# Kernel tuning notes

Hardware: AMD Instinct MI355X
Metric: run time of the kernel (lower is better)

The kernel has to match this reference:

```python
import jax, jax.numpy as jnp
from jax import lax
import numpy as np

H = 256      # encoder_hidden
F = 256      # variance predictor filter_size
K = 3        # kernel_size
NBINS = 256  # variance_embedding n_bins
B, S, T = 64, 512, 2048


def conv1d(x, w, b, pad):
    # x: [B, L, Cin], w: [K, Cin, Cout] -> [B, L, Cout]
    y = lax.conv_general_dilated(x, w, window_strides=(1,), padding=[(pad, pad)],
                                 dimension_numbers=('NWC', 'WIO', 'NWC'))
    return y + b


def layer_norm(x, g, b, eps=1e-5):
    mu = jnp.mean(x, -1, keepdims=True)
    v = jnp.mean((x - mu) ** 2, -1, keepdims=True)
    return (x - mu) * lax.rsqrt(v + eps) * g + b


def predictor(x, mask, w1, b1, g1, be1, w2, b2, g2, be2, lw, lb):
    h = jax.nn.relu(conv1d(x, w1, b1, (K - 1) // 2))
    h = layer_norm(h, g1, be1)
    h = jax.nn.relu(conv1d(h, w2, b2, 1))  # padding=1 hardcoded in original conv1d_2
    h = layer_norm(h, g2, be2)
    out = (h @ lw + lb)[..., 0]            # [B, L]
    return jnp.where(mask, 0.0, out)       # masked_fill(mask, 0.0)


def setup_inputs():
    key = jax.random.key(0)
    ks = jax.random.split(key, 16)
    inp = {
        'x': jax.random.normal(ks[0], (B, S, H), jnp.float32),
        'pitch_target': jax.random.normal(ks[1], (B, S), jnp.float32),
        'energy_target': jax.random.normal(ks[2], (B, S), jnp.float32),
        'src_mask': jnp.zeros((B, S), bool),
        'duration': jax.random.randint(ks[3], (B, S), 0, 4, jnp.int32),
        'max_len': T,
    }
    i = 4
    for p in ['d', 'p', 'e']:
        inp[p + '_w1'] = jax.random.normal(ks[i], (K, H, F), jnp.float32) * 0.05; i += 1
        inp[p + '_b1'] = jnp.zeros((F,), jnp.float32)
        inp[p + '_g1'] = jnp.ones((F,), jnp.float32)
        inp[p + '_be1'] = jnp.zeros((F,), jnp.float32)
        inp[p + '_w2'] = jax.random.normal(ks[i], (K, F, F), jnp.float32) * 0.05; i += 1
        inp[p + '_b2'] = jnp.zeros((F,), jnp.float32)
        inp[p + '_g2'] = jnp.ones((F,), jnp.float32)
        inp[p + '_be2'] = jnp.zeros((F,), jnp.float32)
        inp[p + '_lw'] = jax.random.normal(ks[i], (F, 1), jnp.float32) * 0.05; i += 1
        inp[p + '_lb'] = jnp.zeros((1,), jnp.float32)
    inp['p_table'] = jax.random.normal(ks[i], (NBINS, H), jnp.float32) * 0.02; i += 1
    inp['e_table'] = jax.random.normal(ks[i], (NBINS, H), jnp.float32) * 0.02
    return inp


def reference(x, pitch_target, energy_target, src_mask, duration, max_len,
              d_w1, d_b1, d_g1, d_be1, d_w2, d_b2, d_g2, d_be2, d_lw, d_lb,
              p_w1, p_b1, p_g1, p_be1, p_w2, p_b2, p_g2, p_be2, p_lw, p_lb,
              e_w1, e_b1, e_g1, e_be1, e_w2, e_b2, e_g2, e_be2, e_lw, e_lb,
              p_table, e_table):
    # linear-quantized bins over the data range (stats.json min/max -> [-2, 2] for randn data)
    bins = jnp.linspace(-2.0, 2.0, NBINS - 1, dtype=jnp.float32)

    log_d_pred = predictor(x, src_mask, d_w1, d_b1, d_g1, d_be1, d_w2, d_b2, d_g2, d_be2, d_lw, d_lb)

    # phoneme-level pitch (training path: target given -> embed bucketized target)
    p_pred = predictor(x, src_mask, p_w1, p_b1, p_g1, p_be1, p_w2, p_b2, p_g2, p_be2, p_lw, p_lb)
    p_emb = p_table[jnp.searchsorted(bins, pitch_target, side='left')]  # torch.bucketize(right=False)
    x = x + p_emb

    # phoneme-level energy (predictor runs on x AFTER pitch embedding, as in original)
    e_pred = predictor(x, src_mask, e_w1, e_b1, e_g1, e_be1, e_w2, e_b2, e_g2, e_be2, e_lw, e_lb)
    e_emb = e_table[jnp.searchsorted(bins, energy_target, side='left')]
    x = x + e_emb

    # Length regulation: expand phoneme i duration[b, i] times, pad to max_len.
    cum = jnp.cumsum(duration, axis=1)                 # [B, S]
    mel_len = cum[:, -1]                               # [B]
    frames = jnp.arange(max_len)                       # [T]
    # frame t maps to first phoneme i with cum[i] > t
    idx = jax.vmap(lambda c: jnp.searchsorted(c, frames, side='right'))(cum)  # [B, T]
    idx = jnp.minimum(idx, duration.shape[1] - 1)
    mel = jnp.take_along_axis(x, idx[:, :, None], axis=1)                     # [B, T, H]
    valid = frames[None, :] < mel_len[:, None]
    mel = jnp.where(valid[:, :, None], mel, 0.0)       # zero-pad beyond mel_len

    d_rounded = duration
    return (mel, p_pred, e_pred, log_d_pred, d_rounded, mel_len)
```

## Files before the change

kernel.cpp:

```cpp
#include <hip/hip_runtime.h>
#include <cstdint>
#include <cstddef>


#define HH 256
#define SS 512
#define BB 64
#define TT 2048
#define LSTR 264

typedef __bf16 bf16;
typedef __attribute__((ext_vector_type(8))) __bf16 bf16x8;
typedef __attribute__((ext_vector_type(4))) __bf16 bf16x4;
typedef __attribute__((ext_vector_type(4))) float f32x4;

static constexpr size_t WSZ  = (size_t)3 * HH * HH;
static constexpr size_t H1SZ = (size_t)BB * SS * HH;

__device__ __forceinline__ float edge_val(int j) {
    const float step = 4.0f / 254.0f;
    if (j == 254) return 2.0f;
    return __fadd_rn(-2.0f, __fmul_rn((float)j, step));
}
__device__ __forceinline__ int bucket256(float v) {
    int lo = 0, hi = 255;
    while (lo < hi) {
        int mid = (lo + hi) >> 1;
        if (edge_val(mid) < v) lo = mid + 1; else hi = mid;
    }
    return lo;
}

__global__ void wt_pack(const float* __restrict__ w0, const float* __restrict__ w1,
                        const float* __restrict__ w2, const float* __restrict__ w3,
                        const float* __restrict__ w4, const float* __restrict__ w5,
                        bf16* __restrict__ wp) {
    const int cv = blockIdx.x / 3, k = blockIdx.x % 3;
    const float* wsel[6] = {w0, w1, w2, w3, w4, w5};
    const float* wk = wsel[cv] + (size_t)k * HH * HH;
    bf16* o = wp + ((size_t)(cv * 3 + k)) * HH * HH;
    for (int fb = 0; fb < 16; ++fb) {
        #pragma unroll
        for (int h = 0; h < 2; ++h) {
            const int idx  = threadIdx.x + 256 * h;
            const int kcb  = idx >> 6, lane = idx & 63;
            const int f    = fb * 16 + (lane & 15);
            const int c0   = kcb * 32 + (lane >> 4) * 8;
            bf16x8 v;
            #pragma unroll
            for (int j = 0; j < 8; ++j) v[j] = (bf16)wk[(size_t)(c0 + j) * HH + f];
            *(bf16x8*)(o + (((size_t)fb * 8 + kcb) * 64 + lane) * 8) = v;
        }
    }
}

__global__ __launch_bounds__(256) void xcvt_kernel(
    const float* __restrict__ x, const float* __restrict__ pt,
    const float* __restrict__ ptab,
    bf16* __restrict__ x1, bf16* __restrict__ x2)
{
    const int row = blockIdx.x * 8 + (threadIdx.x >> 5);
    const int c   = (threadIdx.x & 31) * 8;
    const int pb  = bucket256(pt[row]);
    const float4 v0 = *(const float4*)(x + (size_t)row * HH + c);
    const float4 v1 = *(const float4*)(x + (size_t)row * HH + c + 4);
    const float4 t0 = *(const float4*)(ptab + (size_t)pb * HH + c);
    const float4 t1 = *(const float4*)(ptab + (size_t)pb * HH + c + 4);
    bf16x8 a, b2;
    a[0] = (bf16)v0.x; a[1] = (bf16)v0.y; a[2] = (bf16)v0.z; a[3] = (bf16)v0.w;
    a[4] = (bf16)v1.x; a[5] = (bf16)v1.y; a[6] = (bf16)v1.z; a[7] = (bf16)v1.w;
    b2[0] = (bf16)(v0.x + t0.x); b2[1] = (bf16)(v0.y + t0.y);
    b2[2] = (bf16)(v0.z + t0.z); b2[3] = (bf16)(v0.w + t0.w);
    b2[4] = (bf16)(v1.x + t1.x); b2[5] = (bf16)(v1.y + t1.y);
    b2[6] = (bf16)(v1.z + t1.z); b2[7] = (bf16)(v1.w + t1.w);
    *(bf16x8*)(x1 + (size_t)row * HH + c) = a;
    *(bf16x8*)(x2 + (size_t)row * HH + c) = b2;
}

struct Args3 {
    const float* bias[3];
    const float* g[3];
    const float* be[3];
    const float* lw[3];
    const float* lb[3];
    float*       out[3];
};

__global__ __launch_bounds__(256, 3) void conv_fused(
    const bf16* __restrict__ x1,
    const bf16* __restrict__ x2,
    const bf16* __restrict__ wpk,
    Args3 a1, Args3 a2,
    const uint8_t* __restrict__ mask)
{
    __shared__ alignas(16) bf16 tile[82 * LSTR];
    __shared__ float red_s[80][4], red_q[80][4];
    __shared__ float ln_m[80], ln_r[80];

    const int tid    = threadIdx.x;
    const int pred   = blockIdx.x >> 9;
    const int within = blockIdx.x & 511;
    const int b      = within >> 3;
    const int s0     = (within & 7) * 64;

    const int lane = tid & 63;
    const int wv   = tid >> 6;

    const bf16* inb = (pred == 2 ? x2 : x1) + (size_t)b * SS * HH;
    const bf16* wt1 = wpk + (size_t)(pred * 2) * WSZ;
    const bf16* wt2 = wt1 + WSZ;

    for (int idx = tid; idx < 82 * 32; idx += 256) {
        const int r   = idx >> 5, c16 = idx & 31;
        const int s   = s0 - 9 + r;
        bf16x8 v = {};
        if (s >= 0 && s < SS)
            v = *(const bf16x8*)(inb + (size_t)s * HH + c16 * 8);
        *(bf16x8*)&tile[r * LSTR + c16 * 8] = v;
    }
    __syncthreads();

    const int ln15 = lane & 15;
    const int g8   = (lane >> 4) << 3;
    const int q4   = (lane >> 4) << 2;

    f32x4 bini[4];
    #pragma unroll
    for (int mf = 0; mf < 4; ++mf)
        #pragma unroll
        for (int i = 0; i < 4; ++i)
            bini[mf][i] = a1.bias[pred][64 * wv + 16 * mf + q4 + i];

    f32x4 acc1[4][5];
    #pragma unroll
    for (int mf = 0; mf < 4; ++mf)
        #pragma unroll
        for (int sf = 0; sf < 5; ++sf) acc1[mf][sf] = bini[mf];

    #pragma unroll 2
    for (int t = 0; t < 24; ++t) {
        const int k = t >> 3, kcb = t & 7;
        const int kc = kcb << 5;
        bf16x8 aw[4], bx[5];
        const bf16* bp = wt1 + ((((size_t)k * 16 + wv * 4) * 8 + kcb) << 9)
                       + (size_t)lane * 8;
        #pragma unroll
        for (int mf = 0; mf < 4; ++mf)
            aw[mf] = *(const bf16x8*)(bp + ((size_t)mf << 12));
        #pragma unroll
        for (int sf = 0; sf < 5; ++sf)
            bx[sf] = *(const bf16x8*)&tile[(16 * sf + ln15 + k) * LSTR + kc + g8];
        #pragma unroll
        for (int mf = 0; mf < 4; ++mf)
            #pragma unroll
            for (int sf = 0; sf < 5; ++sf)
                acc1[mf][sf] = __builtin_amdgcn_mfma_f32_16x16x32_bf16(
                    aw[mf], bx[sf], acc1[mf][sf], 0, 0, 0);
    }

    #pragma unroll
    for (int mf = 0; mf < 4; ++mf)
        #pragma unroll
        for (int sf = 0; sf < 5; ++sf)
            #pragma unroll
            for (int i = 0; i < 4; ++i)
                acc1[mf][sf][i] = fmaxf(acc1[mf][sf][i], 0.f);

    #pragma unroll
    for (int sf = 0; sf < 5; ++sf) {
        float s = 0.f, q = 0.f;
        #pragma unroll
        for (int mf = 0; mf < 4; ++mf)
            #pragma unroll
            for (int i = 0; i < 4; ++i) {
                const float v = acc1[mf][sf][i];
                s += v; q += v * v;
            }
        s += __shfl_xor(s, 16); s += __shfl_xor(s, 32);
        q += __shfl_xor(q, 16); q += __shfl_xor(q, 32);
        if (lane < 16) { red_s[16 * sf + lane][wv] = s; red_q[16 * sf + lane][wv] = q; }
    }
    __syncthreads();
    if (tid < 80) {
        const float s = red_s[tid][0] + red_s[tid][1] + red_s[tid][2] + red_s[tid][3];
        const float q = red_q[tid][0] + red_q[tid][1] + red_q[tid][2] + red_q[tid][3];
        const float mean = s * (1.f / 256.f);
        const float var  = q * (1.f / 256.f) - mean * mean;
        ln_m[tid] = mean;
        ln_r[tid] = rsqrtf(var + 1e-5f);
    }
    __syncthreads();

    {
        float g1v[4][4], be1v[4][4];
        #pragma unroll
        for (int mf = 0; mf < 4; ++mf)
            #pragma unroll
            for (int i = 0; i < 4; ++i) {
                const int f1 = 64 * wv + 16 * mf + q4 + i;
                g1v[mf][i]  = a1.g[pred][f1];
                be1v[mf][i] = a1.be[pred][f1];
            }
        #pragma unroll
        for (int sf = 0; sf < 5; ++sf) {
            const int o  = 16 * sf + ln15;
            const int hr = o - 7;
            const float mean = ln_m[o], rs = ln_r[o];
            const bool ok = (o >= 7 && o <= 72);
            #pragma unroll
            for (int mf = 0; mf < 4; ++mf) {
                bf16x4 hv;
                #pragma unroll
                for (int i = 0; i < 4; ++i)
                    hv[i] = (bf16)((acc1[mf][sf][i] - mean) * rs * g1v[mf][i] + be1v[mf][i]);
                if (ok)
                    *(bf16x4*)&tile[hr * LSTR + 64 * wv + 16 * mf + q4] = hv;
            }
        }
    }
    __syncthreads();
    if (tid < 64) {
        if (s0 == 0)       *(uint2*)&tile[tid * 4]            = make_uint2(0u, 0u);
        if (s0 == SS - 64) *(uint2*)&tile[65 * LSTR + tid * 4] = make_uint2(0u, 0u);
    }
    __syncthreads();

    #pragma unroll
    for (int mf = 0; mf < 4; ++mf)
        #pragma unroll
        for (int i = 0; i < 4; ++i)
            bini[mf][i] = a2.bias[pred][64 * wv + 16 * mf + q4 + i];

    f32x4 acc2[4][4];
    #pragma unroll
    for (int mf = 0; mf < 4; ++mf)
        #pragma unroll
        for (int sf = 0; sf < 4; ++sf) acc2[mf][sf] = bini[mf];

    #pragma unroll 2
    for (int t = 0; t < 24; ++t) {
        const int k = t >> 3, kcb = t & 7;
        const int kc = kcb << 5;
        bf16x8 aw[4], bx[4];
        const bf16* bp = wt2 + ((((size_t)k * 16 + wv * 4) * 8 + kcb) << 9)
                       + (size_t)lane * 8;
        #pragma unroll
        for (int mf = 0; mf < 4; ++mf)
            aw[mf] = *(const bf16x8*)(bp + ((size_t)mf << 12));
        #pragma unroll
        for (int sf = 0; sf < 4; ++sf)
            bx[sf] = *(const bf16x8*)&tile[(16 * sf + ln15 + k) * LSTR + kc + g8];
        #pragma unroll
        for (int mf = 0; mf < 4; ++mf)
            #pragma unroll
            for (int sf = 0; sf < 4; ++sf)
                acc2[mf][sf] = __builtin_amdgcn_mfma_f32_16x16x32_bf16(
                    aw[mf], bx[sf], acc2[mf][sf], 0, 0, 0);
    }

    #pragma unroll
    for (int mf = 0; mf < 4; ++mf)
        #pragma unroll
        for (int sf = 0; sf < 4; ++sf)
            #pragma unroll
            for (int i = 0; i < 4; ++i)
                acc2[mf][sf][i] = fmaxf(acc2[mf][sf][i], 0.f);

    #pragma unroll
    for (int sf = 0; sf < 4; ++sf) {
        float s = 0.f, q = 0.f;
        #pragma unroll
        for (int mf = 0; mf < 4; ++mf)
            #pragma unroll
            for (int i = 0; i < 4; ++i) {
                const float v = acc2[mf][sf][i];
                s += v; q += v * v;
            }
        s += __shfl_xor(s, 16); s += __shfl_xor(s, 32);
        q += __shfl_xor(q, 16); q += __shfl_xor(q, 32);
        if (lane < 16) { red_s[16 * sf + lane][wv] = s; red_q[16 * sf + lane][wv] = q; }
    }
    __syncthreads();
    if (tid < 64) {
        const float s = red_s[tid][0] + red_s[tid][1] + red_s[tid][2] + red_s[tid][3];
        const float q = red_q[tid][0] + red_q[tid][1] + red_q[tid][2] + red_q[tid][3];
        const float mean = s * (1.f / 256.f);
        const float var  = q * (1.f / 256.f) - mean * mean;
        ln_m[tid] = mean;
        ln_r[tid] = rsqrtf(var + 1e-5f);
    }
    __syncthreads();

    {
        float c1v[4][4], cbv[4][4];
        #pragma unroll
        for (int mf = 0; mf < 4; ++mf)
            #pragma unroll
            for (int i = 0; i < 4; ++i) {
                const int f2 = 64 * wv + 16 * mf + q4 + i;
                const float lwv = a2.lw[pred][f2];
                c1v[mf][i] = a2.g[pred][f2] * lwv;
                cbv[mf][i] = a2.be[pred][f2] * lwv;
            }
        #pragma unroll
        for (int sf = 0; sf < 4; ++sf) {
            const int so = 16 * sf + ln15;
            const float mean = ln_m[so], rs = ln_r[so];
            float t = 0.f;
            #pragma unroll
            for (int mf = 0; mf < 4; ++mf)
                #pragma unroll
                for (int i = 0; i < 4; ++i)
                    t += (acc2[mf][sf][i] - mean) * rs * c1v[mf][i] + cbv[mf][i];
            t += __shfl_xor(t, 16); t += __shfl_xor(t, 32);
            if (lane < 16) red_s[16 * sf + lane][wv] = t;
        }
        __syncthreads();
        if (tid < 64) {
            const int gr = b * SS + s0 + tid;
            const float dv = red_s[tid][0] + red_s[tid][1] + red_s[tid][2] + red_s[tid][3]
                           + a2.lb[pred][0];
            a2.out[pred][gr] = mask[gr] ? 0.f : dv;
        }
    }
}

__global__ void dur_kernel(const int* __restrict__ dur, int* __restrict__ idxb,
                           int* __restrict__ mli,
                           float* __restrict__ drnd, float* __restrict__ mlen) {
    __shared__ int sb[SS];
    const int b = blockIdx.x, t = threadIdx.x;
    const int v = dur[b * SS + t];
    drnd[b * SS + t] = (float)v;
    sb[t] = v;
    __syncthreads();
    for (int off = 1; off < SS; off <<= 1) {
        const int add = (t >= off) ? sb[t - off] : 0;
        __syncthreads();
        sb[t] += add;
        __syncthreads();
    }
    const int hi = sb[t];
    const int lo = hi - v;
    for (int j = lo; j < hi; ++j) idxb[b * TT + j] = t;
    if (t == SS - 1) { mlen[b] = (float)hi; mli[b] = hi; }
}

__global__ __launch_bounds__(256) void gather_kernel(
    const float* __restrict__ x,
    const float* __restrict__ ptab, const float* __restrict__ pt,
    const float* __restrict__ etab, const float* __restrict__ et,
    const int* __restrict__ idxb, const int* __restrict__ mli,
    float* __restrict__ mel)
{
    const int lane = threadIdx.x & 63;
    for (int row = blockIdx.x * 4 + (threadIdx.x >> 6); row < BB * TT; row += 4096 * 4) {
        const int b = row >> 11;
        const int t = row & (TT - 1);
        float4 v = make_float4(0.f, 0.f, 0.f, 0.f);
        if (t < mli[b]) {
            const int idx = idxb[row];
            const size_t src = ((size_t)b * SS + idx) * HH + lane * 4;
            v = *(const float4*)(x + src);
            const int pb = bucket256(pt[b * SS + idx]);
            const int eb = bucket256(et[b * SS + idx]);
            const float4 pv = *(const float4*)(ptab + (size_t)pb * HH + lane * 4);
            const float4 ev = *(const float4*)(etab + (size_t)eb * HH + lane * 4);
            v.x += pv.x + ev.x; v.y += pv.y + ev.y; v.z += pv.z + ev.z; v.w += pv.w + ev.w;
        }
        *(float4*)(mel + (size_t)row * HH + lane * 4) = v;
    }
}

extern "C" void kernel_launch(void* const* d_in, const int* in_sizes, int n_in,
                              void* d_out, int out_size, void* d_ws, size_t ws_size,
                              hipStream_t stream) {
    (void)in_sizes; (void)n_in; (void)out_size; (void)ws_size;

    const float*   x      = (const float*)d_in[0];
    const float*   pitch  = (const float*)d_in[1];
    const float*   energy = (const float*)d_in[2];
    const uint8_t* mask   = (const uint8_t*)d_in[3];
    const int*     dur    = (const int*)d_in[4];
    const float*   ptab   = (const float*)d_in[36];
    const float*   etab   = (const float*)d_in[37];

    float* out = (float*)d_out;
    const size_t N_MEL = (size_t)BB * TT * HH;
    float* out_p  = out + N_MEL;
    float* out_e  = out_p + (size_t)BB * SS;
    float* out_ld = out_e + (size_t)BB * SS;
    float* out_dr = out_ld + (size_t)BB * SS;
    float* out_ml = out_dr + (size_t)BB * SS;

    bf16* wpk  = (bf16*)d_ws;
    int*  idxb = (int*)(wpk + 6 * WSZ);
    int*  mli  = idxb + (size_t)BB * TT;

    bf16* x1 = (bf16*)out;
    bf16* x2 = x1 + H1SZ;

    wt_pack<<<18, 256, 0, stream>>>(
        (const float*)d_in[6],  (const float*)d_in[10],
        (const float*)d_in[16], (const float*)d_in[20],
        (const float*)d_in[26], (const float*)d_in[30],
        wpk);
    xcvt_kernel<<<(BB * SS) / 8, 256, 0, stream>>>(x, pitch, ptab, x1, x2);
    dur_kernel<<<BB, SS, 0, stream>>>(dur, idxb, mli, out_dr, out_ml);

    Args3 a1 = {
        {(const float*)d_in[7],  (const float*)d_in[17], (const float*)d_in[27]},
        {(const float*)d_in[8],  (const float*)d_in[18], (const float*)d_in[28]},
        {(const float*)d_in[9],  (const float*)d_in[19], (const float*)d_in[29]},
        {nullptr, nullptr, nullptr}, {nullptr, nullptr, nullptr},
        {nullptr, nullptr, nullptr}
    };
    Args3 a2 = {
        {(const float*)d_in[11], (const float*)d_in[21], (const float*)d_in[31]},
        {(const float*)d_in[12], (const float*)d_in[22], (const float*)d_in[32]},
        {(const float*)d_in[13], (const float*)d_in[23], (const float*)d_in[33]},
        {(const float*)d_in[14], (const float*)d_in[24], (const float*)d_in[34]},
        {(const float*)d_in[15], (const float*)d_in[25], (const float*)d_in[35]},
        {out_ld, out_p, out_e}
    };

    conv_fused<<<3 * 512, 256, 0, stream>>>(x1, x2, wpk, a1, a2, mask);

    gather_kernel<<<4096, 256, 0, stream>>>(x, ptab, pitch, etab, energy, idxb, mli, out);
}
```

Baseline: 151.0 us.

## Merge prep kernels into one launch, raise MFMA priority, prefetch conv2 weights

Folds the weight packing, duration scan and bf16 conversion kernels into a single launch that dispatches work by block index. This saves two launches and lets the three independent jobs run concurrently. In the conv kernel, MFMA sections are bracketed with s_setprio, and the first weight fragment for the second conv is loaded before the layer-norm epilogue so its latency is hidden. The dur path now uses 256 threads handling two elements each, which adds per-thread scan work.

```diff
diff --git a/kernel.cpp b/kernel.cpp
--- a/kernel.cpp
+++ b/kernel.cpp
@@ -31,50 +31,81 @@
     return lo;
 }
 
-__global__ void wt_pack(const float* __restrict__ w0, const float* __restrict__ w1,
-                        const float* __restrict__ w2, const float* __restrict__ w3,
-                        const float* __restrict__ w4, const float* __restrict__ w5,
-                        bf16* __restrict__ wp) {
-    const int cv = blockIdx.x / 3, k = blockIdx.x % 3;
-    const float* wsel[6] = {w0, w1, w2, w3, w4, w5};
-    const float* wk = wsel[cv] + (size_t)k * HH * HH;
-    bf16* o = wp + ((size_t)(cv * 3 + k)) * HH * HH;
-    for (int fb = 0; fb < 16; ++fb) {
-        #pragma unroll
-        for (int h = 0; h < 2; ++h) {
-            const int idx  = threadIdx.x + 256 * h;
-            const int kcb  = idx >> 6, lane = idx & 63;
-            const int f    = fb * 16 + (lane & 15);
-            const int c0   = kcb * 32 + (lane >> 4) * 8;
-            bf16x8 v;
-            #pragma unroll
-            for (int j = 0; j < 8; ++j) v[j] = (bf16)wk[(size_t)(c0 + j) * HH + f];
-            *(bf16x8*)(o + (((size_t)fb * 8 + kcb) * 64 + lane) * 8) = v;
-        }
-    }
-}
-
-__global__ __launch_bounds__(256) void xcvt_kernel(
+__global__ __launch_bounds__(256) void prep_kernel(
+    const float* __restrict__ w0, const float* __restrict__ w1,
+    const float* __restrict__ w2, const float* __restrict__ w3,
+    const float* __restrict__ w4, const float* __restrict__ w5,
+    bf16* __restrict__ wp,
+    const int* __restrict__ dur, int* __restrict__ idxb, int* __restrict__ mli,
+    float* __restrict__ drnd, float* __restrict__ mlen,
     const float* __restrict__ x, const float* __restrict__ pt,
     const float* __restrict__ ptab,
     bf16* __restrict__ x1, bf16* __restrict__ x2)
 {
-    const int row = blockIdx.x * 8 + (threadIdx.x >> 5);
-    const int c   = (threadIdx.x & 31) * 8;
-    const int pb  = bucket256(pt[row]);
-    const float4 v0 = *(const float4*)(x + (size_t)row * HH + c);
-    const float4 v1 = *(const float4*)(x + (size_t)row * HH + c + 4);
-    const float4 t0 = *(const float4*)(ptab + (size_t)pb * HH + c);
-    const float4 t1 = *(const float4*)(ptab + (size_t)pb * HH + c + 4);
-    bf16x8 a, b2;
-    a[0] = (bf16)v0.x; a[1] = (bf16)v0.y; a[2] = (bf16)v0.z; a[3] = (bf16)v0.w;
-    a[4] = (bf16)v1.x; a[5] = (bf16)v1.y; a[6] = (bf16)v1.z; a[7] = (bf16)v1.w;
-    b2[0] = (bf16)(v0.x + t0.x); b2[1] = (bf16)(v0.y + t0.y);
-    b2[2] = (bf16)(v0.z + t0.z); b2[3] = (bf16)(v0.w + t0.w);
-    b2[4] = (bf16)(v1.x + t1.x); b2[5] = (bf16)(v1.y + t1.y);
-    b2[6] = (bf16)(v1.z + t1.z); b2[7] = (bf16)(v1.w + t1.w);
-    *(bf16x8*)(x1 + (size_t)row * HH + c) = a;
-    *(bf16x8*)(x2 + (size_t)row * HH + c) = b2;
+    const int tid = threadIdx.x;
+    if (blockIdx.x < 18) {
+        const int cv = blockIdx.x / 3, k = blockIdx.x % 3;
+        const float* wsel[6] = {w0, w1, w2, w3, w4, w5};
+        const float* wk = wsel[cv] + (size_t)k * HH * HH;
+        bf16* o = wp + ((size_t)(cv * 3 + k)) * HH * HH;
+        for (int fb = 0; fb < 16; ++fb) {
+            #pragma unroll
+            for (int h = 0; h < 2; ++h) {
+                const int idx  = tid + 256 * h;
+                const int kcb  = idx >> 6, lane = idx & 63;
+                const int f    = fb * 16 + (lane & 15);
+                const int c0   = kcb * 32 + (lane >> 4) * 8;
+                bf16x8 v;
+                #pragma unroll
+                for (int j = 0; j < 8; ++j) v[j] = (bf16)wk[(size_t)(c0 + j) * HH + f];
+                *(bf16x8*)(o + (((size_t)fb * 8 + kcb) * 64 + lane) * 8) = v;
+            }
+        }
+    } else if (blockIdx.x < 82) {
+        __shared__ int sb[SS];
+        const int b = blockIdx.x - 18;
+        const int d0 = dur[b * SS + tid];
+        const int d1 = dur[b * SS + tid + 256];
+        drnd[b * SS + tid]       = (float)d0;
+        drnd[b * SS + tid + 256] = (float)d1;
+        sb[tid]       = d0;
+        sb[tid + 256] = d1;
+        __syncthreads();
+        for (int off = 1; off < SS; off <<= 1) {
+            const int a0 = (tid >= off) ? sb[tid - off] : 0;
+            const int a1 = (tid + 256 >= off) ? sb[tid + 256 - off] : 0;
+            __syncthreads();
+            sb[tid] += a0;
+            sb[tid + 256] += a1;
+            __syncthreads();
+        }
+        {
+            const int hi = sb[tid], lo = hi - d0;
+            for (int j = lo; j < hi; ++j) idxb[b * TT + j] = tid;
+        }
+        {
+            const int hi = sb[tid + 256], lo = hi - d1;
+            for (int j = lo; j < hi; ++j) idxb[b * TT + j] = tid + 256;
+        }
+        if (tid == 255) { mlen[b] = (float)sb[SS - 1]; mli[b] = sb[SS - 1]; }
+    } else {
+        const int row = (blockIdx.x - 82) * 8 + (tid >> 5);
+        const int c   = (tid & 31) * 8;
+        const int pb  = bucket256(pt[row]);
+        const float4 v0 = *(const float4*)(x + (size_t)row * HH + c);
+        const float4 v1 = *(const float4*)(x + (size_t)row * HH + c + 4);
+        const float4 t0 = *(const float4*)(ptab + (size_t)pb * HH + c);
+        const float4 t1 = *(const float4*)(ptab + (size_t)pb * HH + c + 4);
+        bf16x8 a, b2;
+        a[0] = (bf16)v0.x; a[1] = (bf16)v0.y; a[2] = (bf16)v0.z; a[3] = (bf16)v0.w;
+        a[4] = (bf16)v1.x; a[5] = (bf16)v1.y; a[6] = (bf16)v1.z; a[7] = (bf16)v1.w;
+        b2[0] = (bf16)(v0.x + t0.x); b2[1] = (bf16)(v0.y + t0.y);
+        b2[2] = (bf16)(v0.z + t0.z); b2[3] = (bf16)(v0.w + t0.w);
+        b2[4] = (bf16)(v1.x + t1.x); b2[5] = (bf16)(v1.y + t1.y);
+        b2[6] = (bf16)(v1.z + t1.z); b2[7] = (bf16)(v1.w + t1.w);
+        *(bf16x8*)(x1 + (size_t)row * HH + c) = a;
+        *(bf16x8*)(x2 + (size_t)row * HH + c) = b2;
+    }
 }
 
 struct Args3 {
@@ -150,12 +181,22 @@
         #pragma unroll
         for (int sf = 0; sf < 5; ++sf)
             bx[sf] = *(const bf16x8*)&tile[(16 * sf + ln15 + k) * LSTR + kc + g8];
+        __builtin_amdgcn_s_setprio(1);
         #pragma unroll
         for (int mf = 0; mf < 4; ++mf)
             #pragma unroll
             for (int sf = 0; sf < 5; ++sf)
                 acc1[mf][sf] = __builtin_amdgcn_mfma_f32_16x16x32_bf16(
                     aw[mf], bx[sf], acc1[mf][sf], 0, 0, 0);
+        __builtin_amdgcn_s_setprio(0);
+    }
+
+    bf16x8 aw20[4];
+    {
+        const bf16* bp2 = wt2 + (((size_t)wv * 4) * 8 << 9) + (size_t)lane * 8;
+        #pragma unroll
+        for (int mf = 0; mf < 4; ++mf)
+            aw20[mf] = *(const bf16x8*)(bp2 + ((size_t)mf << 12));
     }
 
     #pragma unroll
@@ -237,26 +278,36 @@
         #pragma unroll
         for (int sf = 0; sf < 4; ++sf) acc2[mf][sf] = bini[mf];
 
+#define S2_STEP(AW_, K_, KCB_) do {                                            \
+    const int kc_ = (KCB_) << 5;                                               \
+    bf16x8 bx_[4];                                                             \
+    _Pragma("unroll")                                                          \
+    for (int sf_ = 0; sf_ < 4; ++sf_)                                          \
+        bx_[sf_] = *(const bf16x8*)&tile[(16 * sf_ + ln15 + (K_)) * LSTR       \
+                                         + kc_ + g8];                          \
+    __builtin_amdgcn_s_setprio(1);                                             \
+    _Pragma("unroll")                                                          \
+    for (int mf_ = 0; mf_ < 4; ++mf_)                                          \
+        _Pragma("unroll")                                                      \
+        for (int sf_ = 0; sf_ < 4; ++sf_)                                      \
+            acc2[mf_][sf_] = __builtin_amdgcn_mfma_f32_16x16x32_bf16(          \
+                AW_[mf_], bx_[sf_], acc2[mf_][sf_], 0, 0, 0);                  \
+    __builtin_amdgcn_s_setprio(0);                                             \
+} while (0)
+
+    S2_STEP(aw20, 0, 0);
     #pragma unroll 2
-    for (int t = 0; t < 24; ++t) {
+    for (int t = 1; t < 24; ++t) {
         const int k = t >> 3, kcb = t & 7;
-        const int kc = kcb << 5;
-        bf16x8 aw[4], bx[4];
+        bf16x8 aw[4];
         const bf16* bp = wt2 + ((((size_t)k * 16 + wv * 4) * 8 + kcb) << 9)
                        + (size_t)lane * 8;
         #pragma unroll
         for (int mf = 0; mf < 4; ++mf)
             aw[mf] = *(const bf16x8*)(bp + ((size_t)mf << 12));
-        #pragma unroll
-        for (int sf = 0; sf < 4; ++sf)
-            bx[sf] = *(const bf16x8*)&tile[(16 * sf + ln15 + k) * LSTR + kc + g8];
-        #pragma unroll
-        for (int mf = 0; mf < 4; ++mf)
-            #pragma unroll
-            for (int sf = 0; sf < 4; ++sf)
-                acc2[mf][sf] = __builtin_amdgcn_mfma_f32_16x16x32_bf16(
-                    aw[mf], bx[sf], acc2[mf][sf], 0, 0, 0);
-    }
+        S2_STEP(aw, k, kcb);
+    }
+#undef S2_STEP
 
     #pragma unroll
     for (int mf = 0; mf < 4; ++mf)
@@ -323,27 +374,6 @@
             a2.out[pred][gr] = mask[gr] ? 0.f : dv;
         }
     }
-}
-
-__global__ void dur_kernel(const int* __restrict__ dur, int* __restrict__ idxb,
-                           int* __restrict__ mli,
-                           float* __restrict__ drnd, float* __restrict__ mlen) {
-    __shared__ int sb[SS];
-    const int b = blockIdx.x, t = threadIdx.x;
-    const int v = dur[b * SS + t];
-    drnd[b * SS + t] = (float)v;
-    sb[t] = v;
-    __syncthreads();
-    for (int off = 1; off < SS; off <<= 1) {
-        const int add = (t >= off) ? sb[t - off] : 0;
-        __syncthreads();
-        sb[t] += add;
-        __syncthreads();
-    }
-    const int hi = sb[t];
-    const int lo = hi - v;
-    for (int j = lo; j < hi; ++j) idxb[b * TT + j] = t;
-    if (t == SS - 1) { mlen[b] = (float)hi; mli[b] = hi; }
 }
 
 __global__ __launch_bounds__(256) void gather_kernel(
@@ -400,13 +430,13 @@
     bf16* x1 = (bf16*)out;
     bf16* x2 = x1 + H1SZ;
 
-    wt_pack<<<18, 256, 0, stream>>>(
+    prep_kernel<<<18 + 64 + 4096, 256, 0, stream>>>(
         (const float*)d_in[6],  (const float*)d_in[10],
         (const float*)d_in[16], (const float*)d_in[20],
         (const float*)d_in[26], (const float*)d_in[30],
-        wpk);
-    xcvt_kernel<<<(BB * SS) / 8, 256, 0, stream>>>(x, pitch, ptab, x1, x2);
-    dur_kernel<<<BB, SS, 0, stream>>>(dur, idxb, mli, out_dr, out_ml);
+        wpk,
+        dur, idxb, mli, out_dr, out_ml,
+        x, pitch, ptab, x1, x2);
 
     Args3 a1 = {
         {(const float*)d_in[7],  (const float*)d_in[17], (const float*)d_in[27]},
```

New measurement: 132.2 us, median of 2. 1.14x faster.
